# Kernel tuning notes

Measured on AMD Instinct MI355X. Metric: run time of the kernel, lower is better.

## Reference

```python
import jax, jax.numpy as jnp
import numpy as np

N, E, IN_DIM, HID, OUT = 50000, 600000, 128, 256, 128

def setup_inputs() -> dict:
    key = jax.random.key(0)
    k1, k2, k3, k4, k5, k6, k7 = jax.random.split(key, 7)
    h = jax.random.normal(k1, (N, IN_DIM), dtype=jnp.float32)
    src = jax.random.randint(k2, (E,), 0, N)
    dst = jax.random.randint(k3, (E,), 0, N)
    s1 = 1.0 / np.sqrt(2 * IN_DIM)
    s2 = 1.0 / np.sqrt(HID)
    W1 = jax.random.uniform(k4, (2 * IN_DIM, HID), minval=-s1, maxval=s1, dtype=jnp.float32)
    b1 = jax.random.uniform(k5, (HID,), minval=-s1, maxval=s1, dtype=jnp.float32)
    W2 = jax.random.uniform(k6, (HID, OUT), minval=-s2, maxval=s2, dtype=jnp.float32)
    b2 = jax.random.uniform(k7, (OUT,), minval=-s2, maxval=s2, dtype=jnp.float32)
    return {"h": h, "src": src, "dst": dst, "W1": W1, "b1": b1, "W2": W2, "b2": b2}

def reference(h, src, dst, W1, b1, W2, b2):
    n = h.shape[0]
    # copy_u + mean: gather src features, segment-sum at dst, divide by in-degree
    msg_sum = jax.ops.segment_sum(h[src], dst, num_segments=n)          # [N, D]
    deg = jax.ops.segment_sum(jnp.ones((src.shape[0],), h.dtype), dst, num_segments=n)
    h_neigh = msg_sum / jnp.maximum(deg, 1.0)[:, None]                  # zero-deg nodes -> 0
    h_total = jnp.concatenate([h, h_neigh], axis=1)                     # [N, 2D]
    out = (h_total @ W1 + b1) @ W2 + b2                                 # 2-layer MLP (no inner activation)
    return jax.nn.relu(out)
```

## Files before the change

kernel.cpp:

```cpp
#include <hip/hip_runtime.h>

#define N_NODES 50000
#define E_EDGES 600000
#define IN_DIM  128
#define HID     256
#define OUT_DIM 128
#define CAP     64

#define NB_FILL4 586
#define NB_HCVT8 3125
#define NB_WCVT  384
#define NB_PREP  (NB_FILL4 + NB_HCVT8 + NB_WCVT)
#define NB_MLP   782

typedef __bf16 bf16x8 __attribute__((ext_vector_type(8)));
typedef float  f32x16 __attribute__((ext_vector_type(16)));
typedef unsigned short ushort8 __attribute__((ext_vector_type(8)));

__device__ __forceinline__ unsigned short f2bf(float f) {
    union { float f; unsigned int i; } v; v.f = f;
    unsigned int b = v.i;
    b += 0x7fffu + ((b >> 16) & 1u);
    return (unsigned short)(b >> 16);
}
__device__ __forceinline__ float bf2f(unsigned short u) {
    union { unsigned int i; float f; } v; v.i = ((unsigned int)u) << 16; return v.f;
}

__global__ void __launch_bounds__(256)
sage_prep(const int* __restrict__ src, const int* __restrict__ dst,
          int* __restrict__ counts, char* __restrict__ outb,
          const float* __restrict__ h, unsigned short* __restrict__ ht,
          const float* __restrict__ W1, const float* __restrict__ W2,
          unsigned short* __restrict__ w1sw, unsigned short* __restrict__ w2sw) {
    int b = blockIdx.x;
    if (b < NB_FILL4) {
        int e4 = (b * 256 + threadIdx.x) * 4;
        if (e4 < E_EDGES) {
            const int4 s4 = *(const int4*)(src + e4);
            const int4 d4 = *(const int4*)(dst + e4);
            int sl;
            sl = atomicAdd(counts + d4.x, 1);
            if (sl < CAP) *((int*)(outb + (size_t)d4.x * 512 + 256) + sl) = s4.x;
            sl = atomicAdd(counts + d4.y, 1);
            if (sl < CAP) *((int*)(outb + (size_t)d4.y * 512 + 256) + sl) = s4.y;
            sl = atomicAdd(counts + d4.z, 1);
            if (sl < CAP) *((int*)(outb + (size_t)d4.z * 512 + 256) + sl) = s4.z;
            sl = atomicAdd(counts + d4.w, 1);
            if (sl < CAP) *((int*)(outb + (size_t)d4.w * 512 + 256) + sl) = s4.w;
        }
    } else if (b < NB_FILL4 + NB_HCVT8) {
        int idx = (b - NB_FILL4) * 256 + threadIdx.x;
        int n = idx >> 4, g = idx & 15;
        const float4 v0 = *(const float4*)(h + (size_t)n * IN_DIM + g * 8);
        const float4 v1 = *(const float4*)(h + (size_t)n * IN_DIM + g * 8 + 4);
        ushort8 o;
        o[0] = f2bf(v0.x); o[1] = f2bf(v0.y); o[2] = f2bf(v0.z); o[3] = f2bf(v0.w);
        o[4] = f2bf(v1.x); o[5] = f2bf(v1.y); o[6] = f2bf(v1.z); o[7] = f2bf(v1.w);
        *(ushort8*)(ht + (size_t)n * 128 + g * 8) = o;
    } else {
        int i1 = (b - NB_FILL4 - NB_HCVT8) * 256 + threadIdx.x;
        if (i1 < 65536) {
            int j = i1 & 7, n = (i1 >> 3) & 255, g = (i1 >> 11) & 1, ks = (i1 >> 12) & 3, c = i1 >> 14;
            int k = c * 64 + ks * 16 + g * 8 + j;
            w1sw[i1] = f2bf(W1[(size_t)k * HID + n]);
        } else {
            int i2 = i1 - 65536;
            int j = i2 & 7, n = (i2 >> 3) & 127, g = (i2 >> 10) & 1, ks = (i2 >> 11) & 7, c = (i2 >> 14) & 1;
            int k = c * 128 + ks * 16 + g * 8 + j;
            w2sw[i2] = f2bf(W2[(size_t)k * OUT_DIM + n]);
        }
    }
}

__global__ void __launch_bounds__(256, 4)
sage_fused(const int* __restrict__ counts,
           const unsigned short* __restrict__ ht,
           const unsigned short* __restrict__ w1sw,
           const unsigned short* __restrict__ w2sw,
           const float* __restrict__ b1,
           const float* __restrict__ b2,
           float* out) {
    __shared__ unsigned short hid_s[64][264];

    const int t = threadIdx.x;
    const int nw = t >> 6;
    const int lane = t & 63;
    const int lr = lane & 31;
    const int lg = lane >> 5;
    const int base = blockIdx.x * 64;
    const int row0 = min(base + lr,      N_NODES - 1);
    const int row1 = min(base + 32 + lr, N_NODES - 1);

    {
        int node = base + (t >> 2);
        int l4 = t & 3;
        if (node < N_NODES) {
            int dg = counts[node];
            int entries = min(dg, CAP);
            const int* bk = (const int*)((const char*)out + (size_t)node * 512 + 256);
            float acc[32];
            #pragma unroll
            for (int j = 0; j < 32; ++j) acc[j] = 0.f;
            int4 sx = *(const int4*)(bk);
            int e = 0;
            for (; e + 4 <= entries; e += 4) {
                const int4 nx = *(const int4*)(bk + min(e + 4, CAP - 4));
                const ushort8* p0 = (const ushort8*)(ht + (size_t)sx.x * 128 + l4 * 32);
                const ushort8* p1 = (const ushort8*)(ht + (size_t)sx.y * 128 + l4 * 32);
                const ushort8* p2 = (const ushort8*)(ht + (size_t)sx.z * 128 + l4 * 32);
                const ushort8* p3 = (const ushort8*)(ht + (size_t)sx.w * 128 + l4 * 32);
                ushort8 v00 = p0[0], v01 = p0[1], v02 = p0[2], v03 = p0[3];
                ushort8 v10 = p1[0], v11 = p1[1], v12 = p1[2], v13 = p1[3];
                ushort8 v20 = p2[0], v21 = p2[1], v22 = p2[2], v23 = p2[3];
                ushort8 v30 = p3[0], v31 = p3[1], v32 = p3[2], v33 = p3[3];
                #pragma unroll
                for (int j = 0; j < 8; ++j) {
                    acc[j]      += bf2f(v00[j]) + bf2f(v10[j]) + bf2f(v20[j]) + bf2f(v30[j]);
                    acc[8 + j]  += bf2f(v01[j]) + bf2f(v11[j]) + bf2f(v21[j]) + bf2f(v31[j]);
                    acc[16 + j] += bf2f(v02[j]) + bf2f(v12[j]) + bf2f(v22[j]) + bf2f(v32[j]);
                    acc[24 + j] += bf2f(v03[j]) + bf2f(v13[j]) + bf2f(v23[j]) + bf2f(v33[j]);
                }
                sx = nx;
            }
            for (; e < entries; ++e) {
                const ushort8* p = (const ushort8*)(ht + (size_t)bk[e] * 128 + l4 * 32);
                ushort8 w0 = p[0], w1v = p[1], w2v = p[2], w3 = p[3];
                #pragma unroll
                for (int j = 0; j < 8; ++j) {
                    acc[j]      += bf2f(w0[j]);
                    acc[8 + j]  += bf2f(w1v[j]);
                    acc[16 + j] += bf2f(w2v[j]);
                    acc[24 + j] += bf2f(w3[j]);
                }
            }
            float inv = 1.0f / (float)max(dg, 1);
            int m = t >> 2;
            #pragma unroll
            for (int qq = 0; qq < 4; ++qq) {
                ushort8 o;
                #pragma unroll
                for (int j = 0; j < 8; ++j) o[j] = f2bf(acc[qq * 8 + j] * inv);
                *(ushort8*)(&hid_s[m][l4 * 32 + qq * 8]) = o;
            }
        }
    }

    f32x16 c1[2][2];
    #pragma unroll
    for (int e2 = 0; e2 < 16; ++e2) {
        c1[0][0][e2] = 0.f; c1[0][1][e2] = 0.f; c1[1][0][e2] = 0.f; c1[1][1][e2] = 0.f;
    }

    #pragma unroll
    for (int c = 0; c < 2; ++c) {
        bf16x8 a0[4], a1[4];
        #pragma unroll
        for (int ks = 0; ks < 4; ++ks) {
            int koff = (c * 4 + ks) * 16 + lg * 8;
            a0[ks] = *(const bf16x8*)(ht + (size_t)row0 * 128 + koff);
            a1[ks] = *(const bf16x8*)(ht + (size_t)row1 * 128 + koff);
        }
        #pragma unroll
        for (int ks = 0; ks < 4; ++ks) {
            #pragma unroll
            for (int nt = 0; nt < 2; ++nt) {
                int n = nw * 64 + nt * 32 + lr;
                bf16x8 b = *(const bf16x8*)(w1sw + c * 16384 + (((ks * 2 + lg) * 256) + n) * 8);
                c1[0][nt] = __builtin_amdgcn_mfma_f32_32x32x16_bf16(a0[ks], b, c1[0][nt], 0, 0, 0);
                c1[1][nt] = __builtin_amdgcn_mfma_f32_32x32x16_bf16(a1[ks], b, c1[1][nt], 0, 0, 0);
            }
        }
    }

    __syncthreads();

    #pragma unroll
    for (int c = 2; c < 4; ++c) {
        bf16x8 a0[4], a1[4];
        #pragma unroll
        for (int ks = 0; ks < 4; ++ks) {
            int koff = (c - 2) * 64 + ks * 16 + lg * 8;
            a0[ks] = *(const bf16x8*)(&hid_s[lr][koff]);
            a1[ks] = *(const bf16x8*)(&hid_s[32 + lr][koff]);
        }
        #pragma unroll
        for (int ks = 0; ks < 4; ++ks) {
            #pragma unroll
            for (int nt = 0; nt < 2; ++nt) {
                int n = nw * 64 + nt * 32 + lr;
                bf16x8 b = *(const bf16x8*)(w1sw + c * 16384 + (((ks * 2 + lg) * 256) + n) * 8);
                c1[0][nt] = __builtin_amdgcn_mfma_f32_32x32x16_bf16(a0[ks], b, c1[0][nt], 0, 0, 0);
                c1[1][nt] = __builtin_amdgcn_mfma_f32_32x32x16_bf16(a1[ks], b, c1[1][nt], 0, 0, 0);
            }
        }
    }

    __syncthreads();

    #pragma unroll
    for (int nt = 0; nt < 2; ++nt) {
        int col = nw * 64 + nt * 32 + lr;
        float bias = b1[col];
        #pragma unroll
        for (int s = 0; s < 2; ++s) {
            #pragma unroll
            for (int reg = 0; reg < 16; ++reg) {
                int m = s * 32 + (reg & 3) + 8 * (reg >> 2) + 4 * lg;
                hid_s[m][col] = f2bf(c1[s][nt][reg] + bias);
            }
        }
    }
    __syncthreads();

    f32x16 c2[2];
    #pragma unroll
    for (int e2 = 0; e2 < 16; ++e2) { c2[0][e2] = 0.f; c2[1][e2] = 0.f; }

    #pragma unroll
    for (int c = 0; c < 2; ++c) {
        #pragma unroll
        for (int ks = 0; ks < 8; ++ks) {
            bf16x8 b = *(const bf16x8*)(w2sw + c * 16384 + ((ks * 2 + lg) * 128 + nw * 32 + lr) * 8);
            int koff = c * 128 + ks * 16 + lg * 8;
            bf16x8 ah0 = *(const bf16x8*)(&hid_s[lr][koff]);
            bf16x8 ah1 = *(const bf16x8*)(&hid_s[32 + lr][koff]);
            c2[0] = __builtin_amdgcn_mfma_f32_32x32x16_bf16(ah0, b, c2[0], 0, 0, 0);
            c2[1] = __builtin_amdgcn_mfma_f32_32x32x16_bf16(ah1, b, c2[1], 0, 0, 0);
        }
    }

    {
        int col = nw * 32 + lr;
        float bias = b2[col];
        #pragma unroll
        for (int s = 0; s < 2; ++s) {
            #pragma unroll
            for (int reg = 0; reg < 16; ++reg) {
                int m = s * 32 + (reg & 3) + 8 * (reg >> 2) + 4 * lg;
                int n = base + m;
                if (n < N_NODES)
                    out[(size_t)n * OUT_DIM + col] = fmaxf(c2[s][reg] + bias, 0.0f);
            }
        }
    }
}

extern "C" void kernel_launch(void* const* d_in, const int* in_sizes, int n_in,
                              void* d_out, int out_size, void* d_ws, size_t ws_size,
                              hipStream_t stream) {
    const float* h   = (const float*)d_in[0];
    const int*   src = (const int*)d_in[1];
    const int*   dst = (const int*)d_in[2];
    const float* W1  = (const float*)d_in[3];
    const float* b1  = (const float*)d_in[4];
    const float* W2  = (const float*)d_in[5];
    const float* b2  = (const float*)d_in[6];
    float* out = (float*)d_out;

    int* counts = (int*)d_ws;
    unsigned short* w1sw = (unsigned short*)(counts + N_NODES);
    unsigned short* w2sw = w1sw + 65536;
    unsigned short* ht   = w2sw + 32768;

    hipMemsetAsync(counts, 0, N_NODES * sizeof(int), stream);

    sage_prep<<<NB_PREP, 256, 0, stream>>>(
        src, dst, counts, (char*)d_out, h, ht, W1, W2, w1sw, w2sw);

    sage_fused<<<NB_MLP, 256, 0, stream>>>(counts, ht, w1sw, w2sw, b1, b2, out);
}
```

Baseline: 181.7 us.

## Partition CSR fill by destination range and gather neighbours with whole wavefronts

```diff
diff --git a/kernel.cpp b/kernel.cpp
--- a/kernel.cpp
+++ b/kernel.cpp
@@ -7,11 +7,13 @@
 #define OUT_DIM 128
 #define CAP     64
 
-#define NB_FILL4 586
-#define NB_HCVT8 3125
-#define NB_WCVT  384
-#define NB_PREP  (NB_FILL4 + NB_HCVT8 + NB_WCVT)
-#define NB_MLP   782
+#define RANGE_N 6250
+#define CHUNK_E 2048
+#define NB_FILL 2344
+#define NB_HCVT 3125
+#define NB_WCVT 384
+#define NB_PREP (NB_FILL + NB_HCVT + NB_WCVT)
+#define NB_MLP  782
 
 typedef __bf16 bf16x8 __attribute__((ext_vector_type(8)));
 typedef float  f32x16 __attribute__((ext_vector_type(16)));
@@ -23,8 +25,10 @@
     b += 0x7fffu + ((b >> 16) & 1u);
     return (unsigned short)(b >> 16);
 }
-__device__ __forceinline__ float bf2f(unsigned short u) {
-    union { unsigned int i; float f; } v; v.i = ((unsigned int)u) << 16; return v.f;
+__device__ __forceinline__ void acc2(unsigned u, float& a0, float& a1) {
+    union { unsigned i; float f; } lo, hi;
+    lo.i = u << 16; hi.i = u & 0xffff0000u;
+    a0 += lo.f; a1 += hi.f;
 }
 
 __global__ void __launch_bounds__(256)
@@ -34,23 +38,27 @@
           const float* __restrict__ W1, const float* __restrict__ W2,
           unsigned short* __restrict__ w1sw, unsigned short* __restrict__ w2sw) {
     int b = blockIdx.x;
-    if (b < NB_FILL4) {
-        int e4 = (b * 256 + threadIdx.x) * 4;
-        if (e4 < E_EDGES) {
-            const int4 s4 = *(const int4*)(src + e4);
-            const int4 d4 = *(const int4*)(dst + e4);
-            int sl;
-            sl = atomicAdd(counts + d4.x, 1);
-            if (sl < CAP) *((int*)(outb + (size_t)d4.x * 512 + 256) + sl) = s4.x;
-            sl = atomicAdd(counts + d4.y, 1);
-            if (sl < CAP) *((int*)(outb + (size_t)d4.y * 512 + 256) + sl) = s4.y;
-            sl = atomicAdd(counts + d4.z, 1);
-            if (sl < CAP) *((int*)(outb + (size_t)d4.z * 512 + 256) + sl) = s4.z;
-            sl = atomicAdd(counts + d4.w, 1);
-            if (sl < CAP) *((int*)(outb + (size_t)d4.w * 512 + 256) + sl) = s4.w;
-        }
-    } else if (b < NB_FILL4 + NB_HCVT8) {
-        int idx = (b - NB_FILL4) * 256 + threadIdx.x;
+    if (b < NB_FILL) {
+        int r = b & 7;
+        int chunk = b >> 3;
+        int e0 = chunk * CHUNK_E + threadIdx.x * 8;
+        if (e0 < E_EDGES) {
+            int lo = r * RANGE_N, hi = lo + RANGE_N;
+            const int4 d0 = *(const int4*)(dst + e0);
+            const int4 d1 = *(const int4*)(dst + e0 + 4);
+            int dd[8] = {d0.x, d0.y, d0.z, d0.w, d1.x, d1.y, d1.z, d1.w};
+            #pragma unroll
+            for (int k = 0; k < 8; ++k) {
+                int d = dd[k];
+                if (d >= lo && d < hi) {
+                    int s = src[e0 + k];
+                    int sl = atomicAdd(counts + d, 1);
+                    if (sl < CAP) *((int*)(outb + (size_t)d * 512 + 256) + sl) = s;
+                }
+            }
+        }
+    } else if (b < NB_FILL + NB_HCVT) {
+        int idx = (b - NB_FILL) * 256 + threadIdx.x;
         int n = idx >> 4, g = idx & 15;
         const float4 v0 = *(const float4*)(h + (size_t)n * IN_DIM + g * 8);
         const float4 v1 = *(const float4*)(h + (size_t)n * IN_DIM + g * 8 + 4);
@@ -59,7 +67,7 @@
         o[4] = f2bf(v1.x); o[5] = f2bf(v1.y); o[6] = f2bf(v1.z); o[7] = f2bf(v1.w);
         *(ushort8*)(ht + (size_t)n * 128 + g * 8) = o;
     } else {
-        int i1 = (b - NB_FILL4 - NB_HCVT8) * 256 + threadIdx.x;
+        int i1 = (b - NB_FILL - NB_HCVT) * 256 + threadIdx.x;
         if (i1 < 65536) {
             int j = i1 & 7, n = (i1 >> 3) & 255, g = (i1 >> 11) & 1, ks = (i1 >> 12) & 3, c = i1 >> 14;
             int k = c * 64 + ks * 16 + g * 8 + j;
@@ -93,56 +101,45 @@
     const int row1 = min(base + 32 + lr, N_NODES - 1);
 
     {
-        int node = base + (t >> 2);
-        int l4 = t & 3;
-        if (node < N_NODES) {
+        #pragma unroll 1
+        for (int i = 0; i < 16; ++i) {
+            int m = nw * 16 + i;
+            int node = min(base + m, N_NODES - 1);
             int dg = counts[node];
             int entries = min(dg, CAP);
             const int* bk = (const int*)((const char*)out + (size_t)node * 512 + 256);
-            float acc[32];
-            #pragma unroll
-            for (int j = 0; j < 32; ++j) acc[j] = 0.f;
-            int4 sx = *(const int4*)(bk);
+            float a0 = 0.f, a1 = 0.f;
             int e = 0;
-            for (; e + 4 <= entries; e += 4) {
-                const int4 nx = *(const int4*)(bk + min(e + 4, CAP - 4));
-                const ushort8* p0 = (const ushort8*)(ht + (size_t)sx.x * 128 + l4 * 32);
-                const ushort8* p1 = (const ushort8*)(ht + (size_t)sx.y * 128 + l4 * 32);
-                const ushort8* p2 = (const ushort8*)(ht + (size_t)sx.z * 128 + l4 * 32);
-                const ushort8* p3 = (const ushort8*)(ht + (size_t)sx.w * 128 + l4 * 32);
-                ushort8 v00 = p0[0], v01 = p0[1], v02 = p0[2], v03 = p0[3];
-                ushort8 v10 = p1[0], v11 = p1[1], v12 = p1[2], v13 = p1[3];
-                ushort8 v20 = p2[0], v21 = p2[1], v22 = p2[2], v23 = p2[3];
-                ushort8 v30 = p3[0], v31 = p3[1], v32 = p3[2], v33 = p3[3];
-                #pragma unroll
-                for (int j = 0; j < 8; ++j) {
-                    acc[j]      += bf2f(v00[j]) + bf2f(v10[j]) + bf2f(v20[j]) + bf2f(v30[j]);
-                    acc[8 + j]  += bf2f(v01[j]) + bf2f(v11[j]) + bf2f(v21[j]) + bf2f(v31[j]);
-                    acc[16 + j] += bf2f(v02[j]) + bf2f(v12[j]) + bf2f(v22[j]) + bf2f(v32[j]);
-                    acc[24 + j] += bf2f(v03[j]) + bf2f(v13[j]) + bf2f(v23[j]) + bf2f(v33[j]);
-                }
-                sx = nx;
+            for (; e + 8 <= entries; e += 8) {
+                const int4 q0 = *(const int4*)(bk + e);
+                const int4 q1 = *(const int4*)(bk + e + 4);
+                unsigned u0 = *(const unsigned*)(ht + (size_t)q0.x * 128 + lane * 2);
+                unsigned u1 = *(const unsigned*)(ht + (size_t)q0.y * 128 + lane * 2);
+                unsigned u2 = *(const unsigned*)(ht + (size_t)q0.z * 128 + lane * 2);
+                unsigned u3 = *(const unsigned*)(ht + (size_t)q0.w * 128 + lane * 2);
+                unsigned u4 = *(const unsigned*)(ht + (size_t)q1.x * 128 + lane * 2);
+                unsigned u5 = *(const unsigned*)(ht + (size_t)q1.y * 128 + lane * 2);
+                unsigned u6 = *(const unsigned*)(ht + (size_t)q1.z * 128 + lane * 2);
+                unsigned u7 = *(const unsigned*)(ht + (size_t)q1.w * 128 + lane * 2);
+                acc2(u0, a0, a1); acc2(u1, a0, a1); acc2(u2, a0, a1); acc2(u3, a0, a1);
+                acc2(u4, a0, a1); acc2(u5, a0, a1); acc2(u6, a0, a1); acc2(u7, a0, a1);
+            }
+            if (e + 4 <= entries) {
+                const int4 q = *(const int4*)(bk + e);
+                unsigned u0 = *(const unsigned*)(ht + (size_t)q.x * 128 + lane * 2);
+                unsigned u1 = *(const unsigned*)(ht + (size_t)q.y * 128 + lane * 2);
+                unsigned u2 = *(const unsigned*)(ht + (size_t)q.z * 128 + lane * 2);
+                unsigned u3 = *(const unsigned*)(ht + (size_t)q.w * 128 + lane * 2);
+                acc2(u0, a0, a1); acc2(u1, a0, a1); acc2(u2, a0, a1); acc2(u3, a0, a1);
+                e += 4;
             }
             for (; e < entries; ++e) {
-                const ushort8* p = (const ushort8*)(ht + (size_t)bk[e] * 128 + l4 * 32);
-                ushort8 w0 = p[0], w1v = p[1], w2v = p[2], w3 = p[3];
-                #pragma unroll
-                for (int j = 0; j < 8; ++j) {
-                    acc[j]      += bf2f(w0[j]);
-                    acc[8 + j]  += bf2f(w1v[j]);
-                    acc[16 + j] += bf2f(w2v[j]);
-                    acc[24 + j] += bf2f(w3[j]);
-                }
+                unsigned u = *(const unsigned*)(ht + (size_t)bk[e] * 128 + lane * 2);
+                acc2(u, a0, a1);
             }
             float inv = 1.0f / (float)max(dg, 1);
-            int m = t >> 2;
-            #pragma unroll
-            for (int qq = 0; qq < 4; ++qq) {
-                ushort8 o;
-                #pragma unroll
-                for (int j = 0; j < 8; ++j) o[j] = f2bf(acc[qq * 8 + j] * inv);
-                *(ushort8*)(&hid_s[m][l4 * 32 + qq * 8]) = o;
-            }
+            unsigned o = (unsigned)f2bf(a0 * inv) | ((unsigned)f2bf(a1 * inv) << 16);
+            *(unsigned*)(&hid_s[m][lane * 2]) = o;
         }
     }
 
```

Result: no change. 184.7 us (+1.7%).
